# Optimization experiments

Hardware: AMD Instinct MI355X
Metric: run time of the kernel (lower is better)

## Reference

```python
import jax, jax.numpy as jnp
import numpy as np

B, S, H, NH, DH, L, V, FF = 8, 512, 768, 12, 64, 12, 21128, 3072
PROMPT_LEN = 128
EPS = 1e-12  # BERT LayerNorm eps
NEG = -1e9


def _ln(x, g, b):
    m = jnp.mean(x, axis=-1, keepdims=True)
    xc = x - m
    v = jnp.mean(xc * xc, axis=-1, keepdims=True)
    return xc * jax.lax.rsqrt(v + EPS) * g + b


def setup_inputs() -> dict:
    key = jax.random.key(0)
    ks = jax.random.split(key, 16)
    def p(k, *shape):
        return (jax.random.normal(k, shape, jnp.float32) * 0.02)
    input_ids = jax.random.randint(ks[0], (B, S), 0, V)
    labels = jax.random.randint(ks[1], (B, S), 0, V)
    labels = labels.at[:, :PROMPT_LEN].set(-100)  # prefix = prompt, ignored in CE
    inp = dict(
        input_ids=input_ids,
        labels=labels,
        word_emb=p(ks[2], V, H),
        pos_emb=p(ks[3], S, H),
        type_emb=p(ks[4], 2, H),
        emb_ln_g=jnp.ones((H,), jnp.float32),
        emb_ln_b=jnp.zeros((H,), jnp.float32),
        Wq=p(ks[5], L, H, H), bq=jnp.zeros((L, H), jnp.float32),
        Wk=p(ks[6], L, H, H), bk=jnp.zeros((L, H), jnp.float32),
        Wv=p(ks[7], L, H, H), bv=jnp.zeros((L, H), jnp.float32),
        Wo=p(ks[8], L, H, H), bo=jnp.zeros((L, H), jnp.float32),
        ln1_g=jnp.ones((L, H), jnp.float32), ln1_b=jnp.zeros((L, H), jnp.float32),
        W1=p(ks[9], L, H, FF), bf1=jnp.zeros((L, FF), jnp.float32),
        W2=p(ks[10], L, FF, H), bf2=jnp.zeros((L, H), jnp.float32),
        ln2_g=jnp.ones((L, H), jnp.float32), ln2_b=jnp.zeros((L, H), jnp.float32),
        Wc=p(ks[11], H, V), bc=jnp.zeros((V,), jnp.float32),
    )
    return inp


def _forward(input_ids, labels, word_emb, pos_emb, type_emb, emb_ln_g, emb_ln_b,
             Wq, bq, Wk, bk, Wv, bv, Wo, bo, ln1_g, ln1_b,
             W1, bf1, W2, bf2, ln2_g, ln2_b, Wc, bc):
    # prefix-LM mask: prompt region fully bidirectional-visible, answer region causal
    prompt_len = jnp.sum(labels[0] == -100)
    i = jnp.arange(S)[:, None]
    j = jnp.arange(S)[None, :]
    mask = (j < prompt_len) | ((j >= prompt_len) & (j <= i))  # [S,S]
    bias = jnp.where(mask, 0.0, NEG).astype(jnp.float32)[None, None]  # [1,1,S,S]

    # embeddings (token_type_ids = 0)
    h = word_emb[input_ids] + pos_emb[None, :, :] + type_emb[0][None, None, :]
    h = _ln(h, emb_ln_g, emb_ln_b)
    scale = 1.0 / np.sqrt(DH).astype(np.float32)

    def layer(h, p):
        (wq, bq_, wk, bk_, wv, bv_, wo, bo_, g1, b1_, w1, bff1, w2, bff2, g2, b2_) = p
        q = (h @ wq + bq_).reshape(B, S, NH, DH).transpose(0, 2, 1, 3)
        k = (h @ wk + bk_).reshape(B, S, NH, DH).transpose(0, 2, 1, 3)
        v = (h @ wv + bv_).reshape(B, S, NH, DH).transpose(0, 2, 1, 3)
        scores = jnp.einsum('bhqd,bhkd->bhqk', q, k) * scale + bias
        attn = jax.nn.softmax(scores, axis=-1)
        ctx = jnp.einsum('bhqk,bhkd->bhqd', attn, v)
        ctx = ctx.transpose(0, 2, 1, 3).reshape(B, S, H)
        h = _ln(h + ctx @ wo + bo_, g1, b1_)
        ff = jax.nn.gelu(h @ w1 + bff1, approximate=False) @ w2 + bff2
        h = _ln(h + ff, g2, b2_)
        return h, None

    h, _ = jax.lax.scan(layer, h, (Wq, bq, Wk, bk, Wv, bv, Wo, bo, ln1_g, ln1_b,
                                   W1, bf1, W2, bf2, ln2_g, ln2_b))
    logits = h @ Wc + bc  # [B,S,V]

    # CrossEntropyLoss(ignore_index=-100), mean over valid tokens
    logp = jax.nn.log_softmax(logits, axis=-1)
    valid = labels != -100
    lab = jnp.where(valid, labels, 0)
    nll = -jnp.take_along_axis(logp, lab[..., None], axis=-1)[..., 0]
    loss = jnp.sum(nll * valid) / jnp.sum(valid).astype(jnp.float32)
    return loss


def reference(input_ids, labels, word_emb, pos_emb, type_emb, emb_ln_g, emb_ln_b,
              Wq, bq, Wk, bk, Wv, bv, Wo, bo, ln1_g, ln1_b,
              W1, bf1, W2, bf2, ln2_g, ln2_b, Wc, bc):
    return _forward(input_ids, labels, word_emb, pos_emb, type_emb, emb_ln_g, emb_ln_b,
                    Wq, bq, Wk, bk, Wv, bv, Wo, bo, ln1_g, ln1_b,
                    W1, bf1, W2, bf2, ln2_g, ln2_b, Wc, bc)
```

## Files before the change

kernel.cpp:

```cpp
#include <hip/hip_runtime.h>
#include <hip/hip_bf16.h>
#include <math.h>

#define BB 8
#define SS 512
#define HH 768
#define NHH 12
#define DHH 64
#define LL 12
#define VV 21128
#define VVP 21248
#define FFF 3072
#define TT (BB*SS)
#define PROMPT 128
#define LN_EPS 1e-12f
#define QKVN (3*HH)

typedef __attribute__((ext_vector_type(8))) short short8;
typedef __attribute__((ext_vector_type(4))) short short4v;
typedef __attribute__((ext_vector_type(4))) float floatx4;
typedef __attribute__((ext_vector_type(16))) float floatx16;

__device__ __forceinline__ float gelu_exact(float x) {
    return 0.5f * x * (1.0f + erff(x * 0.70710678118654752f));
}

__device__ __forceinline__ short f2bs(float x) {
    __hip_bfloat16 h = __float2bfloat16(x);
    return *reinterpret_cast<short*>(&h);
}

__device__ __forceinline__ int pack2(float a, float b) {
    const unsigned int lo = (unsigned short)f2bs(a);
    const unsigned int hi = (unsigned short)f2bs(b);
    return (int)(lo | (hi << 16));
}

union I4S8 { int i[4]; short8 s; };

__device__ __forceinline__ void load16_lds(const void* gptr, void* ldsptr) {
    __builtin_amdgcn_global_load_lds(
        (const __attribute__((address_space(1))) unsigned int*)(unsigned long long)(gptr),
        (__attribute__((address_space(3))) unsigned int*)(unsigned long long)(ldsptr),
        16, 0, 0);
}

__global__ __launch_bounds__(256) void gemm_mfma(
    const __hip_bfloat16* __restrict__ A,
    const __hip_bfloat16* __restrict__ Bt,
    const float* __restrict__ bias,
    float* __restrict__ Cf,
    __hip_bfloat16* __restrict__ Ch,
    int M, int N, int K, int act)
{
    __shared__ __hip_bfloat16 As[128 * 32];
    __shared__ __hip_bfloat16 Bs[128 * 32];

    const int tid  = threadIdx.x;
    const int warp = tid >> 6;
    const int row0 = blockIdx.y * 128;
    const int col0 = blockIdx.x * 128;

    const int wm = warp >> 1, wn = warp & 1;
    const int lane = tid & 63;
    const int lr = lane >> 4, lc = lane & 15;

    floatx4 acc[4][4] = {};

    const int sRow = tid >> 2;
    const int sCol = (tid & 3) << 3;
    const __hip_bfloat16* aG0 = A  + (size_t)(row0 + sRow)      * K + sCol;
    const __hip_bfloat16* aG1 = A  + (size_t)(row0 + sRow + 64) * K + sCol;
    const __hip_bfloat16* bG0 = Bt + (size_t)(col0 + sRow)      * K + sCol;
    const __hip_bfloat16* bG1 = Bt + (size_t)(col0 + sRow + 64) * K + sCol;

    char* aL = (char*)As + warp * 1024;
    char* bL = (char*)Bs + warp * 1024;

    for (int k0 = 0; k0 < K; k0 += 32) {
        load16_lds(aG0 + k0, aL);
        load16_lds(aG1 + k0, aL + 4096);
        load16_lds(bG0 + k0, bL);
        load16_lds(bG1 + k0, bL + 4096);
        __syncthreads();

        short8 af[4], bf[4];
        #pragma unroll
        for (int mt = 0; mt < 4; ++mt)
            af[mt] = *(const short8*)((const char*)As + (((wm * 64 + mt * 16 + lc) * 32) + lr * 8) * 2);
        #pragma unroll
        for (int nt = 0; nt < 4; ++nt)
            bf[nt] = *(const short8*)((const char*)Bs + (((wn * 64 + nt * 16 + lc) * 32) + lr * 8) * 2);

        #pragma unroll
        for (int mt = 0; mt < 4; ++mt)
            #pragma unroll
            for (int nt = 0; nt < 4; ++nt)
                acc[mt][nt] = __builtin_amdgcn_mfma_f32_16x16x32_bf16(
                    af[mt], bf[nt], acc[mt][nt], 0, 0, 0);
        __syncthreads();
    }

    #pragma unroll
    for (int mt = 0; mt < 4; ++mt) {
        #pragma unroll
        for (int nt = 0; nt < 4; ++nt) {
            const int n = col0 + wn * 64 + nt * 16 + lc;
            if (n < N) {
                #pragma unroll
                for (int r = 0; r < 4; ++r) {
                    const int m = row0 + wm * 64 + mt * 16 + lr * 4 + r;
                    float v = acc[mt][nt][r];
                    if (bias) v += bias[n];
                    if (act)  v = gelu_exact(v);
                    if (Cf) Cf[(size_t)m * N + n] = v;
                    if (Ch) Ch[(size_t)m * N + n] = __float2bfloat16(v);
                }
            }
        }
    }
}

__global__ void transpose_cvt(
    const float* __restrict__ W, __hip_bfloat16* __restrict__ out,
    int K, int N, long long in_lstride, long long out_lstride,
    int row_off, int out_ld)
{
    __shared__ float t[32][33];
    const int n0 = blockIdx.x * 32;
    const int k0 = blockIdx.y * 32;
    const int z  = blockIdx.z;
    const int tx = threadIdx.x, ty = threadIdx.y;

    const float* Wz = W + (size_t)z * in_lstride;
    __hip_bfloat16* Oz = out + (size_t)z * out_lstride;

    #pragma unroll
    for (int r = 0; r < 4; ++r) {
        const int k = k0 + ty + r * 8;
        const int n = n0 + tx;
        if (k < K && n < N) t[ty + r * 8][tx] = Wz[(size_t)k * N + n];
    }
    __syncthreads();
    #pragma unroll
    for (int r = 0; r < 4; ++r) {
        const int n = n0 + ty + r * 8;
        const int k = k0 + tx;
        if (n < N && k < K)
            Oz[(size_t)(row_off + n) * out_ld + k] = __float2bfloat16(t[tx][ty + r * 8]);
    }
}

__global__ void concat_bias(const float* __restrict__ bq, const float* __restrict__ bk,
                            const float* __restrict__ bv, float* __restrict__ bqkv)
{
    const int i = blockIdx.x * 256 + threadIdx.x;
    if (i >= LL * QKVN) return;
    const int l = i / QKVN, j = i % QKVN;
    float v;
    if (j < HH)            v = bq[l * HH + j];
    else if (j < 2 * HH)   v = bk[l * HH + j - HH];
    else                   v = bv[l * HH + j - 2 * HH];
    bqkv[i] = v;
}

__global__ __launch_bounds__(256) void embed_ln(
    const int* __restrict__ ids, const float* __restrict__ we,
    const float* __restrict__ pe, const float* __restrict__ te,
    const float* __restrict__ g, const float* __restrict__ b,
    __hip_bfloat16* __restrict__ h)
{
    const int t = blockIdx.x;
    const int s = t & (SS - 1);
    const int tid = threadIdx.x;
    __shared__ float x[HH];
    __shared__ float red[256];

    const int id = ids[t];
    for (int j = tid; j < HH; j += 256)
        x[j] = we[(size_t)id * HH + j] + pe[(size_t)s * HH + j] + te[j];
    __syncthreads();

    float sum = x[tid] + x[tid + 256] + x[tid + 512];
    red[tid] = sum; __syncthreads();
    for (int s2 = 128; s2 > 0; s2 >>= 1) { if (tid < s2) red[tid] += red[tid + s2]; __syncthreads(); }
    const float mean = red[0] * (1.0f / HH);
    __syncthreads();

    const float c0 = x[tid] - mean, c1 = x[tid + 256] - mean, c2 = x[tid + 512] - mean;
    red[tid] = c0 * c0 + c1 * c1 + c2 * c2; __syncthreads();
    for (int s2 = 128; s2 > 0; s2 >>= 1) { if (tid < s2) red[tid] += red[tid + s2]; __syncthreads(); }
    const float inv = rsqrtf(red[0] * (1.0f / HH) + LN_EPS);

    h[(size_t)t * HH + tid      ] = __float2bfloat16(c0 * inv * g[tid      ] + b[tid      ]);
    h[(size_t)t * HH + tid + 256] = __float2bfloat16(c1 * inv * g[tid + 256] + b[tid + 256]);
    h[(size_t)t * HH + tid + 512] = __float2bfloat16(c2 * inv * g[tid + 512] + b[tid + 512]);
}

__global__ __launch_bounds__(256) void add_ln(
    const __hip_bfloat16* __restrict__ resid, const float* __restrict__ y,
    const float* __restrict__ g, const float* __restrict__ b,
    __hip_bfloat16* __restrict__ hout)
{
    const int t = blockIdx.x;
    const int tid = threadIdx.x;
    __shared__ float x[HH];
    __shared__ float red[256];

    for (int j = tid; j < HH; j += 256)
        x[j] = __bfloat162float(resid[(size_t)t * HH + j]) + y[(size_t)t * HH + j];
    __syncthreads();

    float sum = x[tid] + x[tid + 256] + x[tid + 512];
    red[tid] = sum; __syncthreads();
    for (int s2 = 128; s2 > 0; s2 >>= 1) { if (tid < s2) red[tid] += red[tid + s2]; __syncthreads(); }
    const float mean = red[0] * (1.0f / HH);
    __syncthreads();

    const float c0 = x[tid] - mean, c1 = x[tid + 256] - mean, c2 = x[tid + 512] - mean;
    red[tid] = c0 * c0 + c1 * c1 + c2 * c2; __syncthreads();
    for (int s2 = 128; s2 > 0; s2 >>= 1) { if (tid < s2) red[tid] += red[tid + s2]; __syncthreads(); }
    const float inv = rsqrtf(red[0] * (1.0f / HH) + LN_EPS);

    hout[(size_t)t * HH + tid      ] = __float2bfloat16(c0 * inv * g[tid      ] + b[tid      ]);
    hout[(size_t)t * HH + tid + 256] = __float2bfloat16(c1 * inv * g[tid + 256] + b[tid + 256]);
    hout[(size_t)t * HH + tid + 512] = __float2bfloat16(c2 * inv * g[tid + 512] + b[tid + 512]);
}

__global__ __launch_bounds__(256) void attn_mfma(
    const float* __restrict__ qkv, __hip_bfloat16* __restrict__ ctx)
{
    const int qb  = blockIdx.x * 128;
    const int hh  = blockIdx.y;
    const int b   = blockIdx.z;
    const int tid = threadIdx.x;
    const int wid = tid >> 6;
    const int lane = tid & 63;
    const int lq = lane & 31;
    const int w  = lane >> 5;

    __shared__ __hip_bfloat16 Kb[64 * 64];
    __shared__ __hip_bfloat16 Vt[64 * 64];

    const int q0 = qb + wid * 32;
    const int i  = q0 + lq;

    short8 qf[4];
    {
        const float* qrow = qkv + (size_t)(b * SS + i) * QKVN + hh * DHH;
        #pragma unroll
        for (int kt = 0; kt < 4; ++kt) {
            const float4 x0 = *(const float4*)(qrow + kt * 16 + w * 8);
            const float4 x1 = *(const float4*)(qrow + kt * 16 + w * 8 + 4);
            short8 q8;
            q8[0] = f2bs(x0.x * 0.125f); q8[1] = f2bs(x0.y * 0.125f);
            q8[2] = f2bs(x0.z * 0.125f); q8[3] = f2bs(x0.w * 0.125f);
            q8[4] = f2bs(x1.x * 0.125f); q8[5] = f2bs(x1.y * 0.125f);
            q8[6] = f2bs(x1.z * 0.125f); q8[7] = f2bs(x1.w * 0.125f);
            qf[kt] = q8;
        }
    }

    floatx16 acc_o[2] = {};
    float m_run = -1e30f, l_run = 0.f;

    const int skey = tid >> 2;
    const int sd4  = (tid & 3) << 2;
    const int vd   = tid & 63;
    const int vk0  = (tid >> 6) << 4;

    const int kmax = (qb + 128 > PROMPT) ? (qb + 128) : PROMPT;

    for (int j0 = 0; j0 < kmax; j0 += 64) {
        {
            const float* kg = qkv + (size_t)(b * SS + j0 + skey) * QKVN + HH + hh * DHH;
            char* krow = (char*)Kb + skey * 128;
            const int sw = (skey & 7) << 4;
            #pragma unroll
            for (int x = 0; x < 4; ++x) {
                const float4 f = *(const float4*)(kg + sd4 + 16 * x);
                short4v kv;
                kv[0] = f2bs(f.x); kv[1] = f2bs(f.y); kv[2] = f2bs(f.z); kv[3] = f2bs(f.w);
                *(short4v*)(krow + (((sd4 << 1) + (x << 5)) ^ sw)) = kv;
            }
        }
        {
            const float* vg = qkv + (size_t)(b * SS + j0 + vk0) * QKVN + 2 * HH + hh * DHH + vd;
            char* vrow = (char*)Vt + vd * 128;
            const int sw = (vd & 7) << 4;
            short8 v8a, v8b;
            #pragma unroll
            for (int x = 0; x < 8; ++x) v8a[x] = f2bs(vg[(size_t)x * QKVN]);
            #pragma unroll
            for (int x = 0; x < 8; ++x) v8b[x] = f2bs(vg[(size_t)(x + 8) * QKVN]);
            *(short8*)(vrow + ((vk0 << 1) ^ sw))        = v8a;
            *(short8*)(vrow + (((vk0 << 1) + 16) ^ sw)) = v8b;
        }
        __syncthreads();

        floatx16 s_acc[2];
        #pragma unroll
        for (int mt = 0; mt < 2; ++mt) {
            const char* krow = (const char*)Kb + (mt * 32 + lq) * 128;
            const int sw = (lq & 7) << 4;
            floatx16 acc = {};
            #pragma unroll
            for (int kt = 0; kt < 4; ++kt) {
                const short8 kf = *(const short8*)(krow + ((kt * 32 + w * 16) ^ sw));
                acc = __builtin_amdgcn_mfma_f32_32x32x16_bf16(kf, qf[kt], acc, 0, 0, 0);
            }
            s_acc[mt] = acc;
        }

        const bool tfull = ((j0 + 63) < PROMPT) || ((j0 + 63) <= q0);
        if (!tfull) {
            #pragma unroll
            for (int mt = 0; mt < 2; ++mt)
                #pragma unroll
                for (int r = 0; r < 16; ++r) {
                    const int key = j0 + mt * 32 + (r & 3) + ((r >> 2) << 3) + (w << 2);
                    if (key >= PROMPT && key > i) s_acc[mt][r] = -1e30f;
                }
        }

        float tmax = -1e30f;
        #pragma unroll
        for (int mt = 0; mt < 2; ++mt)
            #pragma unroll
            for (int r = 0; r < 16; ++r) tmax = fmaxf(tmax, s_acc[mt][r]);
        tmax = fmaxf(tmax, __shfl_xor(tmax, 32, 64));
        const float mnew = fmaxf(m_run, tmax);
        const float corr = __expf(m_run - mnew);
        m_run = mnew;
        float psum = 0.f;
        #pragma unroll
        for (int mt = 0; mt < 2; ++mt)
            #pragma unroll
            for (int r = 0; r < 16; ++r) {
                const float p = __expf(s_acc[mt][r] - mnew);
                s_acc[mt][r] = p;
                psum += p;
            }
        l_run = l_run * corr + psum;
        #pragma unroll
        for (int r = 0; r < 16; ++r) { acc_o[0][r] *= corr; acc_o[1][r] *= corr; }

        short8 pbf[4];
        #pragma unroll
        for (int kt = 0; kt < 4; ++kt) {
            const int mt = kt >> 1;
            const int c0 = ((2 * kt) & 3) << 2;
            const int c1 = ((2 * kt + 1) & 3) << 2;
            const int w0 = pack2(s_acc[mt][c0 + 0], s_acc[mt][c0 + 1]);
            const int w1 = pack2(s_acc[mt][c0 + 2], s_acc[mt][c0 + 3]);
            const int w2 = pack2(s_acc[mt][c1 + 0], s_acc[mt][c1 + 1]);
            const int w3 = pack2(s_acc[mt][c1 + 2], s_acc[mt][c1 + 3]);
            const int t0 = __shfl_xor(w0, 32, 64);
            const int t1 = __shfl_xor(w1, 32, 64);
            const int t2 = __shfl_xor(w2, 32, 64);
            const int t3 = __shfl_xor(w3, 32, 64);
            I4S8 u;
            u.i[0] = w ? t2 : w0;
            u.i[1] = w ? t3 : w1;
            u.i[2] = w ? w2 : t0;
            u.i[3] = w ? w3 : t1;
            pbf[kt] = u.s;
        }

        #pragma unroll
        for (int mtd = 0; mtd < 2; ++mtd) {
            const char* vrow = (const char*)Vt + (mtd * 32 + lq) * 128;
            const int sw = (lq & 7) << 4;
            #pragma unroll
            for (int kt = 0; kt < 4; ++kt) {
                const short8 vf = *(const short8*)(vrow + ((kt * 32 + w * 16) ^ sw));
                acc_o[mtd] = __builtin_amdgcn_mfma_f32_32x32x16_bf16(vf, pbf[kt], acc_o[mtd], 0, 0, 0);
            }
        }
        __syncthreads();
    }

    const float lt  = l_run + __shfl_xor(l_run, 32, 64);
    const float inv = 1.0f / lt;
    __hip_bfloat16* crow = ctx + (size_t)(b * SS + i) * HH + hh * DHH;
    #pragma unroll
    for (int mtd = 0; mtd < 2; ++mtd)
        #pragma unroll
        for (int rq = 0; rq < 4; ++rq) {
            short4v o4;
            #pragma unroll
            for (int e = 0; e < 4; ++e)
                o4[e] = f2bs(acc_o[mtd][rq * 4 + e] * inv);
            *(short4v*)(crow + mtd * 32 + rq * 8 + w * 4) = o4;
        }
}

__global__ __launch_bounds__(256) void ce_kernel(
    const float* __restrict__ logits, const int* __restrict__ labels,
    int bidx, float* __restrict__ acc)
{
    const int r = blockIdx.x;
    const int t = bidx * SS + PROMPT + r;
    const float* row = logits + (size_t)r * VV;
    const int tid = threadIdx.x;
    __shared__ float red[256];

    float mx = -1e30f;
    for (int c = tid; c < VV; c += 256) mx = fmaxf(mx, row[c]);
    red[tid] = mx; __syncthreads();
    for (int s2 = 128; s2 > 0; s2 >>= 1) { if (tid < s2) red[tid] = fmaxf(red[tid], red[tid + s2]); __syncthreads(); }
    mx = red[0];
    __syncthreads();

    float se = 0.f;
    for (int c = tid; c < VV; c += 256) se += __expf(row[c] - mx);
    red[tid] = se; __syncthreads();
    for (int s2 = 128; s2 > 0; s2 >>= 1) { if (tid < s2) red[tid] += red[tid + s2]; __syncthreads(); }

    if (tid == 0) {
        const int lab = labels[t];
        if (lab >= 0) {
            const float nll = -(row[lab] - mx - logf(red[0]));
            atomicAdd(&acc[0], nll);
            atomicAdd(&acc[1], 1.0f);
        }
    }
}

__global__ void finalize_kernel(const float* __restrict__ acc, float* __restrict__ out)
{
    out[0] = (acc[1] > 0.f) ? acc[0] / acc[1] : 0.f;
}

extern "C" void kernel_launch(void* const* d_in, const int* in_sizes, int n_in,
                              void* d_out, int out_size, void* d_ws, size_t ws_size,
                              hipStream_t stream)
{
    const int*   input_ids = (const int*)  d_in[0];
    const int*   labels    = (const int*)  d_in[1];
    const float* word_emb  = (const float*)d_in[2];
    const float* pos_emb   = (const float*)d_in[3];
    const float* type_emb  = (const float*)d_in[4];
    const float* emb_ln_g  = (const float*)d_in[5];
    const float* emb_ln_b  = (const float*)d_in[6];
    const float* Wq = (const float*)d_in[7];   const float* bq = (const float*)d_in[8];
    const float* Wk = (const float*)d_in[9];   const float* bk = (const float*)d_in[10];
    const float* Wv = (const float*)d_in[11];  const float* bv = (const float*)d_in[12];
    const float* Wo = (const float*)d_in[13];  const float* bo = (const float*)d_in[14];
    const float* ln1_g = (const float*)d_in[15]; const float* ln1_b = (const float*)d_in[16];
    const float* W1 = (const float*)d_in[17];  const float* bf1 = (const float*)d_in[18];
    const float* W2 = (const float*)d_in[19];  const float* bf2 = (const float*)d_in[20];
    const float* ln2_g = (const float*)d_in[21]; const float* ln2_b = (const float*)d_in[22];
    const float* Wc = (const float*)d_in[23];  const float* bc = (const float*)d_in[24];

    float* fws = (float*)d_ws;
    float* qkv  = fws;
    float* lg   = qkv;
    float* tmp  = qkv + (size_t)TT * QKVN;
    float* bqkv = tmp + (size_t)TT * HH;
    float* acc  = bqkv + (size_t)LL * QKVN;

    __hip_bfloat16* bws = (__hip_bfloat16*)(acc + 8);
    __hip_bfloat16* h    = bws;
    __hip_bfloat16* ctx  = h    + (size_t)TT * HH;
    __hip_bfloat16* ff1  = ctx  + (size_t)TT * HH;
    __hip_bfloat16* qkvw = ff1  + (size_t)TT * FFF;
    __hip_bfloat16* wot  = qkvw + (size_t)LL * QKVN * HH;
    __hip_bfloat16* w1t  = wot  + (size_t)LL * HH * HH;
    __hip_bfloat16* w2t  = w1t  + (size_t)LL * FFF * HH;
    __hip_bfloat16* wct  = w2t  + (size_t)LL * HH * FFF;

    hipMemsetAsync(acc, 0, 2 * sizeof(float), stream);

    const dim3 tb(32, 8);
    transpose_cvt<<<dim3(24, 24, LL), tb, 0, stream>>>(Wq, qkvw, HH, HH,
        (long long)HH * HH, (long long)QKVN * HH, 0, HH);
    transpose_cvt<<<dim3(24, 24, LL), tb, 0, stream>>>(Wk, qkvw, HH, HH,
        (long long)HH * HH, (long long)QKVN * HH, HH, HH);
    transpose_cvt<<<dim3(24, 24, LL), tb, 0, stream>>>(Wv, qkvw, HH, HH,
        (long long)HH * HH, (long long)QKVN * HH, 2 * HH, HH);
    transpose_cvt<<<dim3(24, 24, LL), tb, 0, stream>>>(Wo, wot, HH, HH,
        (long long)HH * HH, (long long)HH * HH, 0, HH);
    transpose_cvt<<<dim3(96, 24, LL), tb, 0, stream>>>(W1, w1t, HH, FFF,
        (long long)HH * FFF, (long long)FFF * HH, 0, HH);
    transpose_cvt<<<dim3(24, 96, LL), tb, 0, stream>>>(W2, w2t, FFF, HH,
        (long long)FFF * HH, (long long)HH * FFF, 0, FFF);
    transpose_cvt<<<dim3(661, 24, 1), tb, 0, stream>>>(Wc, wct, HH, VV,
        0, 0, 0, HH);
    concat_bias<<<(LL * QKVN + 255) / 256, 256, 0, stream>>>(bq, bk, bv, bqkv);

    embed_ln<<<TT, 256, 0, stream>>>(input_ids, word_emb, pos_emb, type_emb,
                                     emb_ln_g, emb_ln_b, h);

    const dim3 gQKV(QKVN / 128, TT / 128);
    const dim3 gH(HH / 128, TT / 128);
    const dim3 gF(FFF / 128, TT / 128);
    const dim3 gAttn(SS / 128, NHH, BB);

    for (int l = 0; l < LL; ++l) {
        gemm_mfma<<<gQKV, 256, 0, stream>>>(h, qkvw + (size_t)l * QKVN * HH,
            bqkv + (size_t)l * QKVN, qkv, nullptr, TT, QKVN, HH, 0);

        attn_mfma<<<gAttn, 256, 0, stream>>>(qkv, ctx);

        gemm_mfma<<<gH, 256, 0, stream>>>(ctx, wot + (size_t)l * HH * HH,
            bo + (size_t)l * HH, tmp, nullptr, TT, HH, HH, 0);
        add_ln<<<TT, 256, 0, stream>>>(h, tmp, ln1_g + (size_t)l * HH, ln1_b + (size_t)l * HH, h);

        gemm_mfma<<<gF, 256, 0, stream>>>(h, w1t + (size_t)l * FFF * HH,
            bf1 + (size_t)l * FFF, nullptr, ff1, TT, FFF, HH, 1);
        gemm_mfma<<<gH, 256, 0, stream>>>(ff1, w2t + (size_t)l * HH * FFF,
            bf2 + (size_t)l * HH, tmp, nullptr, TT, HH, FFF, 0);
        add_ln<<<TT, 256, 0, stream>>>(h, tmp, ln2_g + (size_t)l * HH, ln2_b + (size_t)l * HH, h);
    }

    const int Mchunk = SS - PROMPT;
    const dim3 gV(VVP / 128, Mchunk / 128);
    for (int b = 0; b < BB; ++b) {
        const __hip_bfloat16* Arow = h + (size_t)(b * SS + PROMPT) * HH;
        gemm_mfma<<<gV, 256, 0, stream>>>(Arow, wct, bc, lg, nullptr, Mchunk, VV, HH, 0);
        ce_kernel<<<Mchunk, 256, 0, stream>>>(lg, labels, b, acc);
    }

    finalize_kernel<<<1, 1, 0, stream>>>(acc, (float*)d_out);
}
```

Baseline: 4.700 ms.

## Deepen GEMM K-tile to 64 with XOR-swizzled LDS and split-K for narrow GEMMs

```diff
diff --git a/kernel.cpp b/kernel.cpp
--- a/kernel.cpp
+++ b/kernel.cpp
@@ -53,51 +53,67 @@
     __hip_bfloat16* __restrict__ Ch,
     int M, int N, int K, int act)
 {
-    __shared__ __hip_bfloat16 As[128 * 32];
-    __shared__ __hip_bfloat16 Bs[128 * 32];
+    __shared__ __hip_bfloat16 As[128 * 64];
+    __shared__ __hip_bfloat16 Bs[128 * 64];
 
     const int tid  = threadIdx.x;
-    const int warp = tid >> 6;
+    const int wid  = tid >> 6;
+    const int lane = tid & 63;
     const int row0 = blockIdx.y * 128;
     const int col0 = blockIdx.x * 128;
 
-    const int wm = warp >> 1, wn = warp & 1;
-    const int lane = tid & 63;
+    const int wm = wid >> 1, wn = wid & 1;
     const int lr = lane >> 4, lc = lane & 15;
 
+    const int nz   = gridDim.z;
+    const int Kc   = K / nz;
+    const int kbeg = blockIdx.z * Kc;
+    if (nz > 1) Cf += (size_t)blockIdx.z * M * N;
+
     floatx4 acc[4][4] = {};
 
-    const int sRow = tid >> 2;
-    const int sCol = (tid & 3) << 3;
-    const __hip_bfloat16* aG0 = A  + (size_t)(row0 + sRow)      * K + sCol;
-    const __hip_bfloat16* aG1 = A  + (size_t)(row0 + sRow + 64) * K + sCol;
-    const __hip_bfloat16* bG0 = Bt + (size_t)(col0 + sRow)      * K + sCol;
-    const __hip_bfloat16* bG1 = Bt + (size_t)(col0 + sRow + 64) * K + sCol;
-
-    char* aL = (char*)As + warp * 1024;
-    char* bL = (char*)Bs + warp * 1024;
-
-    for (int k0 = 0; k0 < K; k0 += 32) {
-        load16_lds(aG0 + k0, aL);
-        load16_lds(aG1 + k0, aL + 4096);
-        load16_lds(bG0 + k0, bL);
-        load16_lds(bG1 + k0, bL + 4096);
+    const int sRow = tid >> 3;
+    const int sC   = (tid & 7) ^ (sRow & 7);
+    const __hip_bfloat16* aG[4];
+    const __hip_bfloat16* bG[4];
+    #pragma unroll
+    for (int p = 0; p < 4; ++p) {
+        aG[p] = A  + (size_t)(row0 + p * 32 + sRow) * K + kbeg + sC * 8;
+        bG[p] = Bt + (size_t)(col0 + p * 32 + sRow) * K + kbeg + sC * 8;
+    }
+    char* aDst = (char*)As + wid * 1024;
+    char* bDst = (char*)Bs + wid * 1024;
+
+    for (int k0 = 0; k0 < Kc; k0 += 64) {
+        #pragma unroll
+        for (int p = 0; p < 4; ++p) {
+            load16_lds(aG[p] + k0, aDst + p * 4096);
+            load16_lds(bG[p] + k0, bDst + p * 4096);
+        }
         __syncthreads();
 
-        short8 af[4], bf[4];
-        #pragma unroll
-        for (int mt = 0; mt < 4; ++mt)
-            af[mt] = *(const short8*)((const char*)As + (((wm * 64 + mt * 16 + lc) * 32) + lr * 8) * 2);
-        #pragma unroll
-        for (int nt = 0; nt < 4; ++nt)
-            bf[nt] = *(const short8*)((const char*)Bs + (((wn * 64 + nt * 16 + lc) * 32) + lr * 8) * 2);
-
-        #pragma unroll
-        for (int mt = 0; mt < 4; ++mt)
-            #pragma unroll
-            for (int nt = 0; nt < 4; ++nt)
-                acc[mt][nt] = __builtin_amdgcn_mfma_f32_16x16x32_bf16(
-                    af[mt], bf[nt], acc[mt][nt], 0, 0, 0);
+        #pragma unroll
+        for (int ks = 0; ks < 2; ++ks) {
+            short8 af[4], bfr[4];
+            #pragma unroll
+            for (int mt = 0; mt < 4; ++mt) {
+                const int row = wm * 64 + mt * 16 + lc;
+                af[mt] = *(const short8*)((const char*)As + row * 128 +
+                         ((((ks << 2) | lr) ^ (row & 7)) << 4));
+            }
+            #pragma unroll
+            for (int nt = 0; nt < 4; ++nt) {
+                const int row = wn * 64 + nt * 16 + lc;
+                bfr[nt] = *(const short8*)((const char*)Bs + row * 128 +
+                          ((((ks << 2) | lr) ^ (row & 7)) << 4));
+            }
+            #pragma unroll
+            for (int mt = 0; mt < 4; ++mt)
+                #pragma unroll
+                for (int nt = 0; nt < 4; ++nt)
+                    acc[mt][nt] = __builtin_amdgcn_mfma_f32_16x16x32_bf16(
+                        af[mt], bfr[nt], acc[mt][nt], 0, 0, 0);
+        }
         __syncthreads();
     }
 
@@ -199,6 +215,7 @@
 
 __global__ __launch_bounds__(256) void add_ln(
     const __hip_bfloat16* __restrict__ resid, const float* __restrict__ y,
+    int P, const float* __restrict__ bias,
     const float* __restrict__ g, const float* __restrict__ b,
     __hip_bfloat16* __restrict__ hout)
 {
@@ -207,8 +224,13 @@
     __shared__ float x[HH];
     __shared__ float red[256];
 
-    for (int j = tid; j < HH; j += 256)
-        x[j] = __bfloat162float(resid[(size_t)t * HH + j]) + y[(size_t)t * HH + j];
+    for (int j = tid; j < HH; j += 256) {
+        float s = __bfloat162float(resid[(size_t)t * HH + j]);
+        if (bias) s += bias[j];
+        for (int p = 0; p < P; ++p)
+            s += y[(size_t)p * TT * HH + (size_t)t * HH + j];
+        x[j] = s;
+    }
     __syncthreads();
 
     float sum = x[tid] + x[tid + 256] + x[tid + 512];
@@ -456,6 +478,7 @@
     float* fws = (float*)d_ws;
     float* qkv  = fws;
     float* lg   = qkv;
+    float* part = qkv;
     float* tmp  = qkv + (size_t)TT * QKVN;
     float* bqkv = tmp + (size_t)TT * HH;
     float* acc  = bqkv + (size_t)LL * QKVN;
@@ -492,9 +515,10 @@
     embed_ln<<<TT, 256, 0, stream>>>(input_ids, word_emb, pos_emb, type_emb,
                                      emb_ln_g, emb_ln_b, h);
 
-    const dim3 gQKV(QKVN / 128, TT / 128);
-    const dim3 gH(HH / 128, TT / 128);
-    const dim3 gF(FFF / 128, TT / 128);
+    const dim3 gQKV(QKVN / 128, TT / 128, 1);
+    const dim3 gWo (HH / 128,  TT / 128, 2);
+    const dim3 gF  (FFF / 128, TT / 128, 1);
+    const dim3 gFF2(HH / 128,  TT / 128, 3);
     const dim3 gAttn(SS / 128, NHH, BB);
 
     for (int l = 0; l < LL; ++l) {
@@ -503,19 +527,22 @@
 
         attn_mfma<<<gAttn, 256, 0, stream>>>(qkv, ctx);
 
-        gemm_mfma<<<gH, 256, 0, stream>>>(ctx, wot + (size_t)l * HH * HH,
-            bo + (size_t)l * HH, tmp, nullptr, TT, HH, HH, 0);
-        add_ln<<<TT, 256, 0, stream>>>(h, tmp, ln1_g + (size_t)l * HH, ln1_b + (size_t)l * HH, h);
+        gemm_mfma<<<gWo, 256, 0, stream>>>(ctx, wot + (size_t)l * HH * HH,
+            nullptr, part, nullptr, TT, HH, HH, 0);
+        add_ln<<<TT, 256, 0, stream>>>(h, part, 2, bo + (size_t)l * HH,
+            ln1_g + (size_t)l * HH, ln1_b + (size_t)l * HH, h);
 
         gemm_mfma<<<gF, 256, 0, stream>>>(h, w1t + (size_t)l * FFF * HH,
             bf1 + (size_t)l * FFF, nullptr, ff1, TT, FFF, HH, 1);
-        gemm_mfma<<<gH, 256, 0, stream>>>(ff1, w2t + (size_t)l * HH * FFF,
-            bf2 + (size_t)l * HH, tmp, nullptr, TT, HH, FFF, 0);
-        add_ln<<<TT, 256, 0, stream>>>(h, tmp, ln2_g + (size_t)l * HH, ln2_b + (size_t)l * HH, h);
+
+        gemm_mfma<<<gFF2, 256, 0, stream>>>(ff1, w2t + (size_t)l * HH * FFF,
+            nullptr, part, nullptr, TT, HH, FFF, 0);
+        add_ln<<<TT, 256, 0, stream>>>(h, part, 3, bf2 + (size_t)l * HH,
+            ln2_g + (size_t)l * HH, ln2_b + (size_t)l * HH, h);
     }
 
     const int Mchunk = SS - PROMPT;
-    const dim3 gV(VVP / 128, Mchunk / 128);
+    const dim3 gV(VVP / 128, Mchunk / 128, 1);
     for (int b = 0; b < BB; ++b) {
         const __hip_bfloat16* Arow = h + (size_t)(b * SS + PROMPT) * HH;
         gemm_mfma<<<gV, 256, 0, stream>>>(Arow, wct, bc, lg, nullptr, Mchunk, VV, HH, 0);
```

Measured after the change: 4.422 ms. 1.06x faster.
